# Kernel optimization log

Measured on AMD Instinct MI355X. Metric: run time of the kernel, lower is better.

The kernel has to match this reference:

```python
import jax, jax.numpy as jnp
import numpy as np

B, S, D = 2, 2048, 4096
NH, NKV, HD = 32, 8, 128
NREP = NH // NKV

def setup_inputs() -> dict:
    key = jax.random.key(0)
    ks = jax.random.split(key, 7)
    sd = 0.02
    return {
        "x": jax.random.normal(ks[0], (B, S, D), dtype=jnp.float32),
        "freqs_cos": jnp.cos(jnp.outer(jnp.arange(S, dtype=jnp.float32), 1.0 / (10000.0 ** (jnp.arange(0, HD, 2, dtype=jnp.float32) / HD)))),
        "freqs_sin": jnp.sin(jnp.outer(jnp.arange(S, dtype=jnp.float32), 1.0 / (10000.0 ** (jnp.arange(0, HD, 2, dtype=jnp.float32) / HD)))),
        "wq": jax.random.normal(ks[1], (D, NH * HD), dtype=jnp.float32) * sd,
        "wk": jax.random.normal(ks[2], (D, NKV * HD), dtype=jnp.float32) * sd,
        "wv": jax.random.normal(ks[3], (D, NKV * HD), dtype=jnp.float32) * sd,
        "wo": jax.random.normal(ks[4], (NH * HD, D), dtype=jnp.float32) * sd,
    }

def _rope(t, cos, sin):
    # t: [b, s, h, hd]; cos/sin: [s, hd/2]
    tr = t.reshape(*t.shape[:-1], -1, 2)
    r, i = tr[..., 0], tr[..., 1]
    c = cos[None, :, None, :]
    s = sin[None, :, None, :]
    out_r = r * c - i * s
    out_i = r * s + i * c
    return jnp.stack([out_r, out_i], axis=-1).reshape(t.shape)

def reference(x, freqs_cos, freqs_sin, wq, wk, wv, wo):
    b, s, _ = x.shape
    xq = (x @ wq).reshape(b, s, NH, HD)
    xk = (x @ wk).reshape(b, s, NKV, HD)
    xv = (x @ wv).reshape(b, s, NKV, HD)
    xq = _rope(xq, freqs_cos, freqs_sin)
    xk = _rope(xk, freqs_cos, freqs_sin)
    # GQA via grouped einsum (equivalent to repeat_kv + SDPA)
    q = xq.transpose(0, 2, 1, 3).reshape(b, NKV, NREP, s, HD)  # [b,g,r,s,d]
    k = xk.transpose(0, 2, 1, 3)  # [b,g,t,d]
    v = xv.transpose(0, 2, 1, 3)
    scale = 1.0 / jnp.sqrt(jnp.float32(HD))
    scores = jnp.einsum('bgrsd,bgtd->bgrst', q, k) * scale
    mask = jnp.where(jnp.triu(jnp.ones((s, s), dtype=bool), 1), -jnp.inf, 0.0).astype(scores.dtype)
    probs = jax.nn.softmax(scores + mask, axis=-1)
    out = jnp.einsum('bgrst,bgtd->bgrsd', probs, v)
    out = out.reshape(b, NH, s, HD).transpose(0, 2, 1, 3).reshape(b, s, NH * HD)
    return out @ wo
```

## Files before the change

### kernel.cpp

```cpp
#include <hip/hip_runtime.h>
#include <hip/hip_bf16.h>
#include <math.h>

typedef __bf16 bf16_t;
typedef __bf16 bf16x4 __attribute__((ext_vector_type(4)));
typedef __bf16 bf16x8 __attribute__((ext_vector_type(8)));
typedef float  f32x4  __attribute__((ext_vector_type(4)));

#define B_   2
#define S_   2048
#define D_   4096
#define NH_  32
#define NKV_ 8
#define HD_  128
#define NREP_ 4
#define QKVN 6144

static __device__ __forceinline__ void gload_lds16(const bf16_t* g, bf16_t* l) {
  __builtin_amdgcn_global_load_lds(
      (const __attribute__((address_space(1))) void*)g,
      (__attribute__((address_space(3))) void*)l, 16, 0, 0);
}

__global__ void convert_f32_bf16(const float* __restrict__ in, bf16_t* __restrict__ out,
                                 size_t n8) {
  size_t i = (size_t)blockIdx.x * blockDim.x + threadIdx.x;
  if (i >= n8) return;
  f32x4 a = *(const f32x4*)(in + i * 8);
  f32x4 b = *(const f32x4*)(in + i * 8 + 4);
  bf16x8 o;
  o[0] = (bf16_t)a[0]; o[1] = (bf16_t)a[1]; o[2] = (bf16_t)a[2]; o[3] = (bf16_t)a[3];
  o[4] = (bf16_t)b[0]; o[5] = (bf16_t)b[1]; o[6] = (bf16_t)b[2]; o[7] = (bf16_t)b[3];
  *(bf16x8*)(out + i * 8) = o;
}

__global__ void transpose_convert(const float* __restrict__ in, bf16_t* __restrict__ out,
                                  int R, int C) {
  __shared__ float tile[32][33];
  const int c0 = blockIdx.x * 32, r0 = blockIdx.y * 32;
  const int tc = threadIdx.x & 31, tr = threadIdx.x >> 5;
#pragma unroll
  for (int i = 0; i < 4; i++) {
    int r = tr + i * 8;
    tile[r][tc] = in[(size_t)(r0 + r) * C + c0 + tc];
  }
  __syncthreads();
#pragma unroll
  for (int i = 0; i < 4; i++) {
    int r = tr + i * 8;
    out[(size_t)(c0 + r) * R + r0 + tc] = (bf16_t)tile[tc][r];
  }
}

__global__ void transpose_v(const bf16_t* __restrict__ qkv, bf16_t* __restrict__ out) {
  __shared__ bf16_t tile[32][33];
  const int t0 = blockIdx.x * 32, d0 = blockIdx.y * 32;
  const int bg = blockIdx.z, b = bg / NKV_, g = bg % NKV_;
  const bf16_t* ibase = qkv + (size_t)b * S_ * QKVN + 5120 + g * HD_;
  bf16_t* obase = out + ((size_t)b * NKV_ + g) * (size_t)HD_ * S_;
  const int tc = threadIdx.x & 31, tr = threadIdx.x >> 5;
#pragma unroll
  for (int i = 0; i < 4; i++) {
    int t = t0 + tr + i * 8;
    tile[tr + i * 8][tc] = ibase[(size_t)t * QKVN + d0 + tc];
  }
  __syncthreads();
#pragma unroll
  for (int i = 0; i < 4; i++) {
    int d = d0 + tr + i * 8;
    obase[(size_t)d * S_ + t0 + tc] = tile[tc][tr + i * 8];
  }
}

__global__ void rope_inplace(bf16_t* __restrict__ x, const float* __restrict__ cosT,
                             const float* __restrict__ sinT, int lgh, size_t nchunks) {
  size_t i = (size_t)blockIdx.x * blockDim.x + threadIdx.x;
  if (i >= nchunks) return;
  const int d8 = (int)(i & 15);
  const int h = (int)((i >> 4) & ((1u << lgh) - 1));
  const size_t pos = i >> (4 + lgh);
  const int s = (int)(pos & (S_ - 1));
  bf16_t* p = x + pos * QKVN + h * HD_ + d8 * 8;
  bf16x8 v = *(bf16x8*)p;
  f32x4 c  = *(const f32x4*)(cosT + (size_t)s * 64 + d8 * 4);
  f32x4 sn = *(const f32x4*)(sinT + (size_t)s * 64 + d8 * 4);
  bf16x8 o;
#pragma unroll
  for (int j = 0; j < 4; j++) {
    float re = (float)v[2 * j], im = (float)v[2 * j + 1];
    o[2 * j]     = (bf16_t)(re * c[j] - im * sn[j]);
    o[2 * j + 1] = (bf16_t)(re * sn[j] + im * c[j]);
  }
  *(bf16x8*)p = o;
}

template <typename OutT>
__global__ __launch_bounds__(512, 2) void gemm8p(const bf16_t* __restrict__ Ag,
                                                 const bf16_t* __restrict__ Bg,
                                                 OutT* __restrict__ C,
                                                 int M, int N, int K) {
  extern __shared__ __align__(16) bf16_t lds[];
  const int t = threadIdx.x;
  const int w = t >> 6, l = t & 63;
  const int wm = w >> 2, wn = w & 3;
  const int lr = l & 15, lg = l >> 4;

  const int nbx = gridDim.x;
  const int nwg = nbx * gridDim.y;
  const int bid = blockIdx.y * nbx + blockIdx.x;
  const int cpx = nwg >> 3;
  const int sid = (bid & 7) * cpx + (bid >> 3);
  const int n0 = (sid % nbx) * 256;
  const int m0 = (sid / nbx) * 256;

  const int srow = t >> 3;
  const int colsw = ((t & 7) ^ (srow & 7)) * 8;
  const int xsw = (lr & 7) * 8;

  auto stageA = [&](int db, int k0, int q) {
    gload_lds16(Ag + (size_t)(m0 + q * 64 + srow) * K + k0 + colsw,
                lds + db * 32768 + q * 4096 + t * 8);
  };
  auto stageB = [&](int db, int k0, int q) {
    gload_lds16(Bg + (size_t)(n0 + q * 64 + srow) * K + k0 + colsw,
                lds + db * 32768 + 16384 + q * 4096 + t * 8);
  };

  f32x4 acc[8][4];
  const f32x4 zero = {0.f, 0.f, 0.f, 0.f};
#pragma unroll
  for (int m = 0; m < 8; m++)
#pragma unroll
    for (int n = 0; n < 4; n++) acc[m][n] = zero;

  const int KT = K >> 6;

#pragma unroll
  for (int q = 0; q < 4; q++) stageA(0, 0, q);
#pragma unroll
  for (int q = 0; q < 4; q++) stageB(0, 0, q);
#pragma unroll
  for (int q = 0; q < 4; q++) stageB(1, 64, q);
  stageA(1, 64, 0);
  stageA(1, 64, 2);
  asm volatile("s_waitcnt vmcnt(6)" ::: "memory");
  __builtin_amdgcn_s_barrier();

  for (int c = 0; c < KT; ++c) {
    const int d = c & 1;
    const bf16_t* pA = lds + d * 32768;
    const bf16_t* pB = pA + 16384;
    const bool st2 = (c + 2) < KT;
    const int k2 = (c + 2) << 6;
    bf16x8 bfrag[4][2];

#pragma unroll
    for (int p = 0; p < 4; ++p) {
      if (p == 0) {
#pragma unroll
        for (int n = 0; n < 4; n++)
#pragma unroll
          for (int ks = 0; ks < 2; ks++)
            bfrag[n][ks] =
                *(const bf16x8*)(pB + (wn * 64 + n * 16 + lr) * 64 + ((ks * 32 + lg * 8) ^ xsw));
      }
      bf16x8 a0 = *(const bf16x8*)(pA + (wm * 128 + (2 * p) * 16 + lr) * 64 + ((lg * 8) ^ xsw));
      bf16x8 a1 = *(const bf16x8*)(pA + (wm * 128 + (2 * p) * 16 + lr) * 64 + ((32 + lg * 8) ^ xsw));
      bf16x8 a2 = *(const bf16x8*)(pA + (wm * 128 + (2 * p + 1) * 16 + lr) * 64 + ((lg * 8) ^ xsw));
      bf16x8 a3 = *(const bf16x8*)(pA + (wm * 128 + (2 * p + 1) * 16 + lr) * 64 + ((32 + lg * 8) ^ xsw));

      if (p == 0) {
        if (c + 1 < KT) { stageA(1 - d, (c + 1) << 6, 1); stageA(1 - d, (c + 1) << 6, 3); }
      } else if (p == 1) {
        if (st2) { stageB(d, k2, 0); stageB(d, k2, 1); }
      } else if (p == 2) {
        if (st2) { stageB(d, k2, 2); stageB(d, k2, 3); }
      } else {
        if (st2) { stageA(d, k2, 0); stageA(d, k2, 2); }
      }

      if (p == 0) asm volatile("s_waitcnt lgkmcnt(8)" ::: "memory");
      __builtin_amdgcn_s_barrier();
      asm volatile("s_waitcnt lgkmcnt(0)" ::: "memory");
      __builtin_amdgcn_sched_barrier(0);

      __builtin_amdgcn_s_setprio(1);
#pragma unroll
      for (int n = 0; n < 4; n++) {
        acc[2 * p][n]     = __builtin_amdgcn_mfma_f32_16x16x32_bf16(a0, bfrag[n][0], acc[2 * p][n], 0, 0, 0);
        acc[2 * p][n]     = __builtin_amdgcn_mfma_f32_16x16x32_bf16(a1, bfrag[n][1], acc[2 * p][n], 0, 0, 0);
        acc[2 * p + 1][n] = __builtin_amdgcn_mfma_f32_16x16x32_bf16(a2, bfrag[n][0], acc[2 * p + 1][n], 0, 0, 0);
        acc[2 * p + 1][n] = __builtin_amdgcn_mfma_f32_16x16x32_bf16(a3, bfrag[n][1], acc[2 * p + 1][n], 0, 0, 0);
      }
      __builtin_amdgcn_s_setprio(0);

      if (p == 3) {
        if (st2) asm volatile("s_waitcnt vmcnt(6)" ::: "memory");
        else     asm volatile("s_waitcnt vmcnt(0)" ::: "memory");
      }
      __builtin_amdgcn_s_barrier();
    }
  }

#pragma unroll
  for (int m = 0; m < 8; m++)
#pragma unroll
    for (int n = 0; n < 4; n++) {
      const int row = m0 + wm * 128 + m * 16 + lg * 4;
      const int col = n0 + wn * 64 + n * 16 + lr;
#pragma unroll
      for (int r = 0; r < 4; r++) C[(size_t)(row + r) * N + col] = (OutT)acc[m][n][r];
    }
}

#define QBLK 128
#define KVBLK 64
__global__ __launch_bounds__(256, 2) void flash_attn3(const bf16_t* __restrict__ QKV,
                                                      const bf16_t* __restrict__ Vt,
                                                      bf16_t* __restrict__ O) {
  const int pair = blockIdx.x;
  const int h = blockIdx.y, b = blockIdx.z;
  const int g = h >> 2;
  const int t = threadIdx.x, w = t >> 6, l = t & 63;
  const int lr = l & 15, lg = l >> 4;

  __shared__ __align__(16) char lds[49152];
  char* Ks = lds;
  char* Vs = lds + 16384;
  char* Ps = lds + 32768 + w * 4096;

  const float scale = 0.08838834764831845f;
  const int xm = (lr & 7) << 4;

  for (int phase = 0; phase < 2; phase++) {
    const int qtile = phase ? (15 - pair) : pair;
    const int q0 = qtile * QBLK;
    const int wq = q0 + w * 32;

    bf16x8 qreg[2][4];
#pragma unroll
    for (int qt = 0; qt < 2; qt++)
#pragma unroll
      for (int kk = 0; kk < 4; kk++) {
        bf16x8 v = *(const bf16x8*)&QKV[((size_t)b * S_ + wq + qt * 16 + lr) * QKVN +
                                        h * HD_ + kk * 32 + lg * 8];
#pragma unroll
        for (int j = 0; j < 8; j++) v[j] = (bf16_t)((float)v[j] * scale);
        qreg[qt][kk] = v;
      }

    float mrun[2] = {-INFINITY, -INFINITY};
    float lrun[2] = {0.f, 0.f};
    f32x4 acc[2][8];
    const f32x4 zero = {0.f, 0.f, 0.f, 0.f};
#pragma unroll
    for (int qt = 0; qt < 2; qt++)
#pragma unroll
      for (int d = 0; d < 8; d++) acc[qt][d] = zero;

    const int nkb = (q0 + QBLK) >> 6;
    for (int kb = 0; kb < nkb; kb++) {
      const int t0 = kb * KVBLK;
      __syncthreads();
#pragma unroll
      for (int i = 0; i < 4; i++) {
        const int c = t + i * 256;
        const int row = c >> 4, sl = c & 15;
        bf16x8 kv = *(const bf16x8*)&QKV[((size_t)b * S_ + t0 + row) * QKVN + 4096 +
                                         g * HD_ + sl * 8];
        *(bf16x8*)(Ks + row * 256 + ((sl * 16) ^ ((row & 7) << 4))) = kv;
      }
#pragma unroll
      for (int i = 0; i < 4; i++) {
        const int c = t + i * 256;
        const int row = c >> 3, sl = c & 7;
        bf16x8 vv = *(const bf16x8*)&Vt[(((size_t)b * NKV_ + g) * HD_ + row) * S_ + t0 + sl * 8];
        *(bf16x8*)(Vs + row * 128 + ((sl * 16) ^ ((row & 7) << 4))) = vv;
      }
      __syncthreads();

      if (t0 > wq + 31) continue;

      f32x4 st[4][2];
#pragma unroll
      for (int n = 0; n < 4; n++) { st[n][0] = zero; st[n][1] = zero; }
#pragma unroll
      for (int kk = 0; kk < 4; kk++) {
        const int colb = (kk * 64 + lg * 16) ^ xm;
#pragma unroll
        for (int n = 0; n < 4; n++) {
          const bf16x8 ak = *(const bf16x8*)(Ks + (n * 16 + lr) * 256 + colb);
          st[n][0] = __builtin_amdgcn_mfma_f32_16x16x32_bf16(ak, qreg[0][kk], st[n][0], 0, 0, 0);
          st[n][1] = __builtin_amdgcn_mfma_f32_16x16x32_bf16(ak, qreg[1][kk], st[n][1], 0, 0, 0);
        }
      }

      const bool needmask = (t0 + KVBLK - 1 > wq);
#pragma unroll
      for (int qt = 0; qt < 2; qt++) {
        const int q = wq + qt * 16 + lr;
        if (needmask) {
#pragma unroll
          for (int n = 0; n < 4; n++)
#pragma unroll
            for (int r = 0; r < 4; r++)
              if (t0 + n * 16 + lg * 4 + r > q) st[n][qt][r] = -INFINITY;
        }
        float mx = -INFINITY;
#pragma unroll
        for (int n = 0; n < 4; n++)
#pragma unroll
          for (int r = 0; r < 4; r++) mx = fmaxf(mx, st[n][qt][r]);
        mx = fmaxf(mx, __shfl_xor(mx, 16));
        mx = fmaxf(mx, __shfl_xor(mx, 32));
        const float mnew = fmaxf(mrun[qt], mx);
        const float corr = __expf(mrun[qt] - mnew);
        mrun[qt] = mnew;
        float sum = 0.f;
        bf16x4 pk[4];
#pragma unroll
        for (int n = 0; n < 4; n++) {
#pragma unroll
          for (int r = 0; r < 4; r++) {
            const float p = __expf(st[n][qt][r] - mnew);
            sum += p;
            pk[n][r] = (bf16_t)p;
          }
        }
        sum += __shfl_xor(sum, 16);
        sum += __shfl_xor(sum, 32);
        lrun[qt] = lrun[qt] * corr + sum;
        {
          char* pbase = Ps + (qt * 16 + lr) * 128;
#pragma unroll
          for (int n = 0; n < 4; n++)
            *(bf16x4*)(pbase + ((n * 32 + lg * 8) ^ xm)) = pk[n];
        }
#pragma unroll
        for (int r = 0; r < 4; r++) {
          const float cb = __shfl(corr, lg * 4 + r);
#pragma unroll
          for (int db = 0; db < 8; db++) acc[qt][db][r] *= cb;
        }
      }

#pragma unroll
      for (int kk = 0; kk < 2; kk++) {
        const int colb = (kk * 64 + lg * 16) ^ xm;
        const bf16x8 ap0 = *(const bf16x8*)(Ps + lr * 128 + colb);
        const bf16x8 ap1 = *(const bf16x8*)(Ps + (16 + lr) * 128 + colb);
#pragma unroll
        for (int db = 0; db < 8; db++) {
          const bf16x8 bv = *(const bf16x8*)(Vs + (db * 16 + lr) * 128 + colb);
          acc[0][db] = __builtin_amdgcn_mfma_f32_16x16x32_bf16(ap0, bv, acc[0][db], 0, 0, 0);
          acc[1][db] = __builtin_amdgcn_mfma_f32_16x16x32_bf16(ap1, bv, acc[1][db], 0, 0, 0);
        }
      }
    }

#pragma unroll
    for (int qt = 0; qt < 2; qt++) {
      const float linv = 1.f / lrun[qt];
#pragma unroll
      for (int r = 0; r < 4; r++) {
        const float li = __shfl(linv, lg * 4 + r);
        const int q = wq + qt * 16 + lg * 4 + r;
#pragma unroll
        for (int db = 0; db < 8; db++)
          O[(((size_t)b * S_ + q) * NH_ + h) * HD_ + db * 16 + lr] = (bf16_t)(acc[qt][db][r] * li);
      }
    }
    __syncthreads();
  }
}

extern "C" void kernel_launch(void* const* d_in, const int* in_sizes, int n_in,
                              void* d_out, int out_size, void* d_ws, size_t ws_size,
                              hipStream_t stream) {
  const float* x    = (const float*)d_in[0];
  const float* fcos = (const float*)d_in[1];
  const float* fsin = (const float*)d_in[2];
  const float* wq   = (const float*)d_in[3];
  const float* wk   = (const float*)d_in[4];
  const float* wv   = (const float*)d_in[5];
  const float* wo   = (const float*)d_in[6];
  float* out = (float*)d_out;

  char* ws = (char*)d_ws;
  bf16_t* x_bf   = (bf16_t*)(ws);
  bf16_t* wqkvT  = (bf16_t*)(ws + 33554432);
  bf16_t* qkv    = (bf16_t*)(ws + 83886080);
  bf16_t* vt     = (bf16_t*)(ws + 134217728);
  bf16_t* attn   = (bf16_t*)(ws + 142606336);

  hipFuncSetAttribute(reinterpret_cast<const void*>(gemm8p<bf16_t>),
                      hipFuncAttributeMaxDynamicSharedMemorySize, 131072);
  hipFuncSetAttribute(reinterpret_cast<const void*>(gemm8p<float>),
                      hipFuncAttributeMaxDynamicSharedMemorySize, 131072);

  convert_f32_bf16<<<8192, 256, 0, stream>>>(x, x_bf, (size_t)2097152);
  transpose_convert<<<dim3(128, 128), 256, 0, stream>>>(wq, wqkvT, 4096, 4096);
  transpose_convert<<<dim3(32, 128), 256, 0, stream>>>(wk, wqkvT + (size_t)4096 * 4096, 4096, 1024);
  transpose_convert<<<dim3(32, 128), 256, 0, stream>>>(wv, wqkvT + (size_t)5120 * 4096, 4096, 1024);
  gemm8p<bf16_t><<<dim3(24, 16), 512, 131072, stream>>>(x_bf, wqkvT, qkv, 4096, QKVN, 4096);
  rope_inplace<<<8192, 256, 0, stream>>>(qkv, fcos, fsin, 5, (size_t)2097152);
  rope_inplace<<<2048, 256, 0, stream>>>(qkv + 4096, fcos, fsin, 3, (size_t)524288);
  transpose_v<<<dim3(64, 4, 16), 256, 0, stream>>>(qkv, vt);
  transpose_convert<<<dim3(128, 128), 256, 0, stream>>>(wo, wqkvT, 4096, 4096);
  flash_attn3<<<dim3(8, 32, 2), 256, 0, stream>>>(qkv, vt, attn);
  gemm8p<float><<<dim3(16, 16), 512, 131072, stream>>>(attn, wqkvT, out, 4096, 4096, 4096);
}
```

Baseline: 530.9 us.

## Software-pipeline GEMM LDS fragment reads and fuse Q RoPE into attention

The GEMM main loop is restructured so the A fragments for the next phase are read from LDS while the current phase's MFMAs run. Ping-pong register sets (aE/aO) replace the per-phase lgkmcnt(0) waits, and the next tile's first A fragment is prefetched across the loop boundary. Separately, the RoPE rotation of Q is moved into the flash attention Q load, which drops the standalone rope kernel pass over the Q region. The cost is more live registers, a changed vmcnt wait count that must still cover the pending loads, and Q RoPE rounded through bf16 once instead of twice.

```diff
diff --git a/kernel.cpp b/kernel.cpp
--- a/kernel.cpp
+++ b/kernel.cpp
@@ -133,6 +133,42 @@
 #pragma unroll
     for (int n = 0; n < 4; n++) acc[m][n] = zero;
 
+  bf16x8 bfrag[4][2];
+  bf16x8 aE[4], aO[4];
+
+  auto readA = [&](bf16x8* dst, const bf16_t* base, int p) {
+    const bf16_t* r0 = base + (wm * 128 + (2 * p) * 16 + lr) * 64;
+    const bf16_t* r1 = base + (wm * 128 + (2 * p + 1) * 16 + lr) * 64;
+    dst[0] = *(const bf16x8*)(r0 + ((lg * 8) ^ xsw));
+    dst[1] = *(const bf16x8*)(r0 + ((32 + lg * 8) ^ xsw));
+    dst[2] = *(const bf16x8*)(r1 + ((lg * 8) ^ xsw));
+    dst[3] = *(const bf16x8*)(r1 + ((32 + lg * 8) ^ xsw));
+  };
+  auto readB = [&](const bf16_t* pB) {
+#pragma unroll
+    for (int n = 0; n < 4; n++)
+#pragma unroll
+      for (int ks = 0; ks < 2; ks++)
+        bfrag[n][ks] =
+            *(const bf16x8*)(pB + (wn * 64 + n * 16 + lr) * 64 + ((ks * 32 + lg * 8) ^ xsw));
+  };
+  auto mfmaPhase = [&](int p, const bf16x8* a) {
+    __builtin_amdgcn_s_setprio(1);
+#pragma unroll
+    for (int n = 0; n < 4; n++)
+      acc[2 * p][n] = __builtin_amdgcn_mfma_f32_16x16x32_bf16(a[0], bfrag[n][0], acc[2 * p][n], 0, 0, 0);
+#pragma unroll
+    for (int n = 0; n < 4; n++)
+      acc[2 * p + 1][n] = __builtin_amdgcn_mfma_f32_16x16x32_bf16(a[2], bfrag[n][0], acc[2 * p + 1][n], 0, 0, 0);
+#pragma unroll
+    for (int n = 0; n < 4; n++)
+      acc[2 * p][n] = __builtin_amdgcn_mfma_f32_16x16x32_bf16(a[1], bfrag[n][1], acc[2 * p][n], 0, 0, 0);
+#pragma unroll
+    for (int n = 0; n < 4; n++)
+      acc[2 * p + 1][n] = __builtin_amdgcn_mfma_f32_16x16x32_bf16(a[3], bfrag[n][1], acc[2 * p + 1][n], 0, 0, 0);
+    __builtin_amdgcn_s_setprio(0);
+  };
+
   const int KT = K >> 6;
 
 #pragma unroll
@@ -145,6 +181,8 @@
   stageA(1, 64, 2);
   asm volatile("s_waitcnt vmcnt(6)" ::: "memory");
   __builtin_amdgcn_s_barrier();
+  __builtin_amdgcn_sched_barrier(0);
+  readA(aE, lds, 0);
 
   for (int c = 0; c < KT; ++c) {
     const int d = c & 1;
@@ -152,54 +190,33 @@
     const bf16_t* pB = pA + 16384;
     const bool st2 = (c + 2) < KT;
     const int k2 = (c + 2) << 6;
-    bf16x8 bfrag[4][2];
-
-#pragma unroll
-    for (int p = 0; p < 4; ++p) {
-      if (p == 0) {
-#pragma unroll
-        for (int n = 0; n < 4; n++)
-#pragma unroll
-          for (int ks = 0; ks < 2; ks++)
-            bfrag[n][ks] =
-                *(const bf16x8*)(pB + (wn * 64 + n * 16 + lr) * 64 + ((ks * 32 + lg * 8) ^ xsw));
-      }
-      bf16x8 a0 = *(const bf16x8*)(pA + (wm * 128 + (2 * p) * 16 + lr) * 64 + ((lg * 8) ^ xsw));
-      bf16x8 a1 = *(const bf16x8*)(pA + (wm * 128 + (2 * p) * 16 + lr) * 64 + ((32 + lg * 8) ^ xsw));
-      bf16x8 a2 = *(const bf16x8*)(pA + (wm * 128 + (2 * p + 1) * 16 + lr) * 64 + ((lg * 8) ^ xsw));
-      bf16x8 a3 = *(const bf16x8*)(pA + (wm * 128 + (2 * p + 1) * 16 + lr) * 64 + ((32 + lg * 8) ^ xsw));
-
-      if (p == 0) {
-        if (c + 1 < KT) { stageA(1 - d, (c + 1) << 6, 1); stageA(1 - d, (c + 1) << 6, 3); }
-      } else if (p == 1) {
-        if (st2) { stageB(d, k2, 0); stageB(d, k2, 1); }
-      } else if (p == 2) {
-        if (st2) { stageB(d, k2, 2); stageB(d, k2, 3); }
-      } else {
-        if (st2) { stageA(d, k2, 0); stageA(d, k2, 2); }
-      }
-
-      if (p == 0) asm volatile("s_waitcnt lgkmcnt(8)" ::: "memory");
-      __builtin_amdgcn_s_barrier();
-      asm volatile("s_waitcnt lgkmcnt(0)" ::: "memory");
-      __builtin_amdgcn_sched_barrier(0);
-
-      __builtin_amdgcn_s_setprio(1);
-#pragma unroll
-      for (int n = 0; n < 4; n++) {
-        acc[2 * p][n]     = __builtin_amdgcn_mfma_f32_16x16x32_bf16(a0, bfrag[n][0], acc[2 * p][n], 0, 0, 0);
-        acc[2 * p][n]     = __builtin_amdgcn_mfma_f32_16x16x32_bf16(a1, bfrag[n][1], acc[2 * p][n], 0, 0, 0);
-        acc[2 * p + 1][n] = __builtin_amdgcn_mfma_f32_16x16x32_bf16(a2, bfrag[n][0], acc[2 * p + 1][n], 0, 0, 0);
-        acc[2 * p + 1][n] = __builtin_amdgcn_mfma_f32_16x16x32_bf16(a3, bfrag[n][1], acc[2 * p + 1][n], 0, 0, 0);
-      }
-      __builtin_amdgcn_s_setprio(0);
-
-      if (p == 3) {
-        if (st2) asm volatile("s_waitcnt vmcnt(6)" ::: "memory");
-        else     asm volatile("s_waitcnt vmcnt(0)" ::: "memory");
-      }
-      __builtin_amdgcn_s_barrier();
-    }
+
+    readB(pB);
+    readA(aO, pA, 1);
+    if (c + 1 < KT) { stageA(1 - d, (c + 1) << 6, 1); stageA(1 - d, (c + 1) << 6, 3); }
+    mfmaPhase(0, aE);
+    __builtin_amdgcn_s_barrier();
+    __builtin_amdgcn_sched_barrier(0);
+
+    readA(aE, pA, 2);
+    if (st2) { stageB(d, k2, 0); stageB(d, k2, 1); }
+    mfmaPhase(1, aO);
+    __builtin_amdgcn_s_barrier();
+    __builtin_amdgcn_sched_barrier(0);
+
+    readA(aO, pA, 3);
+    if (st2) { stageB(d, k2, 2); stageB(d, k2, 3); }
+    mfmaPhase(2, aE);
+    if (st2) asm volatile("s_waitcnt vmcnt(4)" ::: "memory");
+    else     asm volatile("s_waitcnt vmcnt(0)" ::: "memory");
+    __builtin_amdgcn_s_barrier();
+    __builtin_amdgcn_sched_barrier(0);
+
+    if (c + 1 < KT) readA(aE, lds + (1 - d) * 32768, 0);
+    if (st2) { stageA(d, k2, 0); stageA(d, k2, 2); }
+    mfmaPhase(3, aO);
+    __builtin_amdgcn_s_barrier();
+    __builtin_amdgcn_sched_barrier(0);
   }
 
 #pragma unroll
@@ -217,6 +234,8 @@
 #define KVBLK 64
 __global__ __launch_bounds__(256, 2) void flash_attn3(const bf16_t* __restrict__ QKV,
                                                       const bf16_t* __restrict__ Vt,
+                                                      const float* __restrict__ cosT,
+                                                      const float* __restrict__ sinT,
                                                       bf16_t* __restrict__ O) {
   const int pair = blockIdx.x;
   const int h = blockIdx.y, b = blockIdx.z;
@@ -239,15 +258,24 @@
 
     bf16x8 qreg[2][4];
 #pragma unroll
-    for (int qt = 0; qt < 2; qt++)
+    for (int qt = 0; qt < 2; qt++) {
+      const int s = wq + qt * 16 + lr;
 #pragma unroll
       for (int kk = 0; kk < 4; kk++) {
-        bf16x8 v = *(const bf16x8*)&QKV[((size_t)b * S_ + wq + qt * 16 + lr) * QKVN +
+        bf16x8 v = *(const bf16x8*)&QKV[((size_t)b * S_ + s) * QKVN +
                                         h * HD_ + kk * 32 + lg * 8];
-#pragma unroll
-        for (int j = 0; j < 8; j++) v[j] = (bf16_t)((float)v[j] * scale);
-        qreg[qt][kk] = v;
-      }
+        f32x4 c4 = *(const f32x4*)(cosT + (size_t)s * 64 + kk * 16 + lg * 4);
+        f32x4 s4 = *(const f32x4*)(sinT + (size_t)s * 64 + kk * 16 + lg * 4);
+        bf16x8 o;
+#pragma unroll
+        for (int j = 0; j < 4; j++) {
+          float re = (float)v[2 * j], im = (float)v[2 * j + 1];
+          o[2 * j]     = (bf16_t)((re * c4[j] - im * s4[j]) * scale);
+          o[2 * j + 1] = (bf16_t)((re * s4[j] + im * c4[j]) * scale);
+        }
+        qreg[qt][kk] = o;
+      }
+    }
 
     float mrun[2] = {-INFINITY, -INFINITY};
     float lrun[2] = {0.f, 0.f};
@@ -403,10 +431,9 @@
   transpose_convert<<<dim3(32, 128), 256, 0, stream>>>(wk, wqkvT + (size_t)4096 * 4096, 4096, 1024);
   transpose_convert<<<dim3(32, 128), 256, 0, stream>>>(wv, wqkvT + (size_t)5120 * 4096, 4096, 1024);
   gemm8p<bf16_t><<<dim3(24, 16), 512, 131072, stream>>>(x_bf, wqkvT, qkv, 4096, QKVN, 4096);
-  rope_inplace<<<8192, 256, 0, stream>>>(qkv, fcos, fsin, 5, (size_t)2097152);
   rope_inplace<<<2048, 256, 0, stream>>>(qkv + 4096, fcos, fsin, 3, (size_t)524288);
   transpose_v<<<dim3(64, 4, 16), 256, 0, stream>>>(qkv, vt);
   transpose_convert<<<dim3(128, 128), 256, 0, stream>>>(wo, wqkvT, 4096, 4096);
-  flash_attn3<<<dim3(8, 32, 2), 256, 0, stream>>>(qkv, vt, attn);
+  flash_attn3<<<dim3(8, 32, 2), 256, 0, stream>>>(qkv, vt, fcos, fsin, attn);
   gemm8p<float><<<dim3(16, 16), 512, 131072, stream>>>(attn, wqkvT, out, 4096, 4096, 4096);
 }
```

Measured after the change: 512.4 us. 1.04x faster.
